# Kernel tuning notes

Measured on AMD Instinct MI355X. Metric: run time of the kernel, lower is better.

Reference implementation:

```python
import jax, jax.numpy as jnp
import numpy as np

B, T, H = 2, 2048, 1024
DFF = 4 * H        # dense_mlp hidden width
E = 8              # num_experts_temp
TOP_K = 2


def setup_inputs() -> dict:
    key = jax.random.key(0)
    ks = jax.random.split(key, 6)
    s_h = 1.0 / np.sqrt(H)
    s_f = 1.0 / np.sqrt(DFF)
    return {
        "hidden_states": jax.random.normal(ks[0], (B, T, H), dtype=jnp.float32),
        "router_w": jax.random.normal(ks[1], (E, H), dtype=jnp.float32) * s_h,
        "w1": jax.random.normal(ks[2], (E, H, DFF), dtype=jnp.float32) * s_h,
        "b1": jnp.zeros((E, DFF), dtype=jnp.float32),
        "w2": jax.random.normal(ks[3], (E, DFF, H), dtype=jnp.float32) * s_f,
        "b2": jnp.zeros((E, H), dtype=jnp.float32),
    }


def reference(hidden_states, router_w, w1, b1, w2, b2):
    # Router: [B,T,E]
    router_logits = jnp.einsum("bth,eh->bte", hidden_states, router_w)
    topk_vals, topk_idx = jax.lax.top_k(router_logits, TOP_K)        # [B,T,K]
    topk_w = jax.nn.softmax(topk_vals.astype(jnp.float32), axis=-1)
    topk_w = topk_w.astype(hidden_states.dtype)

    # Dense compute of ALL experts (faithful to the original module).
    h = jnp.einsum("bth,ehf->btef", hidden_states, w1) + b1          # [B,T,E,DFF]
    h = jax.nn.gelu(h)
    expert_out = jnp.einsum("btef,efh->bteh", h, w2) + b2            # [B,T,E,H]

    # Gather top-k experts per token and mix.
    topk_out = jnp.take_along_axis(expert_out, topk_idx[..., None], axis=2)  # [B,T,K,H]
    mixed = jnp.sum(topk_out * topk_w[..., None], axis=2)            # [B,T,H]
    return mixed
```

## Files before the change

### kernel.cpp

```cpp
#include <hip/hip_runtime.h>
#include <hip/hip_bf16.h>
#include <stdint.h>

#define AS1 __attribute__((address_space(1)))
#define AS3 __attribute__((address_space(3)))

typedef __bf16 bf16x8 __attribute__((ext_vector_type(8)));
typedef float floatx4 __attribute__((ext_vector_type(4)));

static constexpr int NTOK = 4096;
static constexpr int H    = 1024;
static constexpr int DFF  = 4096;
static constexpr int E    = 8;
static constexpr int BN   = 128;
static constexpr int RBMAX = 72;

static constexpr size_t OFF_WS     = 0;
static constexpr size_t OFF_XCS    = 67108864;
static constexpr size_t OFF_HS     = 85983232;
static constexpr size_t OFF_P1     = 161480704;
static constexpr size_t OFF_RTIDX  = 180355072;
static constexpr size_t OFF_RTW    = 180387840;
static constexpr size_t OFF_PTOK   = 180420608;
static constexpr size_t OFF_PW     = 180457472;
static constexpr size_t OFF_TOKPOS = 180494336;
static constexpr size_t OFF_CNT    = 180527104;
static constexpr size_t WS_NEED    = 180527232;

__device__ __forceinline__ unsigned short f2bf(float f) {
    __bf16 b = (__bf16)f;
    return __builtin_bit_cast(unsigned short, b);
}
__device__ __forceinline__ float bf2f(unsigned short u) {
    unsigned int v = ((unsigned int)u) << 16;
    return __builtin_bit_cast(float, v);
}

__device__ __forceinline__ void gload16(const void* g, void* l) {
    __builtin_amdgcn_global_load_lds((AS1 void*)g, (AS3 void*)l, 16, 0, 0);
}

__global__ __launch_bounds__(256) void k_router(const float* __restrict__ x,
                                                const float* __restrict__ rw,
                                                int* __restrict__ rt_idx,
                                                float* __restrict__ rt_w,
                                                int* __restrict__ counts) {
    const int wv = threadIdx.x >> 6, ln = threadIdx.x & 63;
    const int t = blockIdx.x * 4 + wv;
    const float* xr = x + (size_t)t * H + ln * 4;
    float4 xv[4];
#pragma unroll
    for (int c = 0; c < 4; ++c) xv[c] = *(const float4*)(xr + c * 256);
    float lg[E];
#pragma unroll
    for (int e = 0; e < E; ++e) {
        const float* rr = rw + (size_t)e * H + ln * 4;
        float acc = 0.f;
#pragma unroll
        for (int c = 0; c < 4; ++c) {
            float4 rv = *(const float4*)(rr + c * 256);
            acc += xv[c].x * rv.x + xv[c].y * rv.y + xv[c].z * rv.z + xv[c].w * rv.w;
        }
#pragma unroll
        for (int s = 32; s > 0; s >>= 1) acc += __shfl_xor(acc, s, 64);
        lg[e] = acc;
    }
    if (ln == 0) {
        int i0 = 0; float v0 = lg[0];
#pragma unroll
        for (int e = 1; e < E; ++e) if (lg[e] > v0) { v0 = lg[e]; i0 = e; }
        int i1 = -1; float v1 = -INFINITY;
#pragma unroll
        for (int e = 0; e < E; ++e) if (e != i0 && lg[e] > v1) { v1 = lg[e]; i1 = e; }
        float e1 = expf(v1 - v0);
        float inv = 1.f / (1.f + e1);
        rt_idx[2 * t] = i0; rt_idx[2 * t + 1] = i1;
        rt_w[2 * t] = inv;  rt_w[2 * t + 1] = e1 * inv;
        atomicAdd(&counts[i0], 1);
        atomicAdd(&counts[i1], 1);
    }
}

__global__ void k_offsets(const int* __restrict__ counts, int* __restrict__ offs) {
    if (threadIdx.x == 0) {
        int o = 0;
        for (int e = 0; e < E; ++e) { offs[e] = o; o += (counts[e] + 127) & ~127; }
        offs[E] = o;
    }
}

__global__ __launch_bounds__(256) void k_scatter(const int* __restrict__ rt_idx,
                                                 const float* __restrict__ rt_w,
                                                 const int* __restrict__ offs,
                                                 int* __restrict__ cursors,
                                                 int* __restrict__ pair_tok,
                                                 float* __restrict__ pair_w,
                                                 int* __restrict__ tok_pos) {
    int t = blockIdx.x * 256 + threadIdx.x;
    if (t >= NTOK) return;
    for (int k = 0; k < 2; ++k) {
        int e = rt_idx[2 * t + k];
        int p = atomicAdd(&cursors[e], 1);
        int pos = offs[e] + p;
        pair_tok[pos] = t;
        pair_w[pos] = rt_w[2 * t + k];
        tok_pos[2 * t + k] = pos;
    }
}

__global__ __launch_bounds__(256) void k_gather(const float* __restrict__ x,
                                                const int* __restrict__ offs,
                                                const int* __restrict__ counts,
                                                const int* __restrict__ pair_tok,
                                                unsigned short* __restrict__ xcs) {
    int pos = blockIdx.x;
    if (pos >= offs[E]) return;
    int e = 0;
    while (e < E - 1 && pos >= offs[e + 1]) ++e;
    bool valid = (pos - offs[e]) < counts[e];
    int tok = valid ? pair_tok[pos] : 0;
    int k0 = threadIdx.x * 4;
    float4 xv = valid ? *(const float4*)(x + (size_t)tok * H + k0)
                      : make_float4(0.f, 0.f, 0.f, 0.f);
    ushort4 o;
    o.x = f2bf(xv.x); o.y = f2bf(xv.y); o.z = f2bf(xv.z); o.w = f2bf(xv.w);
    int rb = pos >> 7, m = pos & 127;
    size_t idx = (((size_t)(rb * 32 + (k0 >> 5)) * 128 + m) * 32) + (((k0 >> 3) & 3) << 3) + (k0 & 7);
    *(ushort4*)(xcs + idx) = o;
}

template <int K, int N>
__global__ __launch_bounds__(256) void k_convert(const float* __restrict__ w,
                                                 unsigned short* __restrict__ ws) {
    constexpr int KB = K / 32, NB = N / 64;
    int bid = blockIdx.x;
    int nb = bid % NB, kb = (bid / NB) % KB, e = bid / (NB * KB);
    int kq = threadIdx.x & 3, nl = threadIdx.x >> 2;
    int n = nb * 64 + nl;
    const float* src = w + ((size_t)e * K + kb * 32 + kq * 8) * N + n;
    union { unsigned short us[8]; uint4 v; } u;
#pragma unroll
    for (int j = 0; j < 8; ++j) u.us[j] = f2bf(src[(size_t)j * N]);
    size_t oct = ((size_t)(e * KB + kb) * N + n) * 4 + kq;
    *(uint4*)(ws + oct * 8) = u.v;
}

__global__ __launch_bounds__(256) void k_gemm1(const unsigned short* __restrict__ Xc,
                                               const unsigned short* __restrict__ W1s,
                                               const int* __restrict__ offs,
                                               const float* __restrict__ b1,
                                               unsigned short* __restrict__ Hs) {
    constexpr int KB = H / 32;
    constexpr int MP = 36;
    const int rb = blockIdx.y;
    if (rb * 128 >= offs[E]) return;
    int e = 0;
    while (e < E - 1 && rb * 128 >= offs[e + 1]) ++e;
    const int n0 = blockIdx.x * BN;

    __shared__ unsigned short smem[4 * 128 * MP];
    unsigned short* lds_a = smem;
    unsigned short* lds_b = smem + 4096;

    const int tid = threadIdx.x;
    const int wv = tid >> 6, ln = tid & 63;
    const int quad = ln >> 4, lr = ln & 15;
    const int wm = (wv & 1) * 64, wn = (wv >> 1) * 64;

    floatx4 acc[4][4];
#pragma unroll
    for (int i = 0; i < 4; ++i)
#pragma unroll
        for (int j = 0; j < 4; ++j) acc[i][j] = (floatx4){0.f, 0.f, 0.f, 0.f};

    const unsigned short* Atile = Xc + (size_t)rb * KB * 4096;
    const unsigned short* Btile = W1s + ((size_t)e * KB * DFF + n0) * 32;

    for (int kb = 0; kb < KB; ++kb) {
        __syncthreads();
        const unsigned short* a_src = Atile + (size_t)kb * 4096 + (wv * 2) * 512 + ln * 8;
        const unsigned short* b_src = Btile + (size_t)kb * DFF * 32 + (wv * 2) * 512 + ln * 8;
#pragma unroll
        for (int c = 0; c < 2; ++c) {
            gload16(a_src + c * 512, &lds_a[(wv * 2 + c) * 512]);
            gload16(b_src + c * 512, &lds_b[(wv * 2 + c) * 512]);
        }
        __syncthreads();
        bf16x8 af[4], bg[4];
#pragma unroll
        for (int i = 0; i < 4; ++i) {
            af[i] = *(const bf16x8*)(lds_a + (wm + i * 16 + lr) * 32 + quad * 8);
            bg[i] = *(const bf16x8*)(lds_b + (wn + i * 16 + lr) * 32 + quad * 8);
        }
#pragma unroll
        for (int i = 0; i < 4; ++i)
#pragma unroll
            for (int j = 0; j < 4; ++j)
                acc[i][j] = __builtin_amdgcn_mfma_f32_16x16x32_bf16(af[i], bg[j], acc[i][j], 0, 0, 0);
    }

    float bj[4];
#pragma unroll
    for (int j = 0; j < 4; ++j) bj[j] = b1[(size_t)e * DFF + n0 + wn + j * 16 + lr];
    __syncthreads();
#pragma unroll
    for (int j = 0; j < 4; ++j) {
        const int fl = wn + j * 16 + lr;
        const int fb = fl >> 5, f5 = fl & 31;
        unsigned short* dst = smem + fb * (128 * MP) + f5;
#pragma unroll
        for (int i = 0; i < 4; ++i) {
#pragma unroll
            for (int r = 0; r < 4; ++r) {
                const int m = wm + i * 16 + quad * 4 + r;
                float v = acc[i][j][r] + bj[j];
                float u = 0.79788456080286535588f * (v + 0.044715f * v * v * v);
                float ez = __expf(2.f * u);
                float g = v * (1.f - 1.f / (ez + 1.f));
                dst[m * MP] = f2bf(g);
            }
        }
    }
    __syncthreads();
    const size_t hsbase = ((size_t)rb * 128 + (n0 >> 5)) * 4096;
#pragma unroll
    for (int it = 0; it < 8; ++it) {
        const int g = (it * 256 + tid) * 8;
        const int fb = g >> 12, rem = g & 4095, m = rem >> 5, f5 = rem & 31;
        const unsigned short* s = smem + fb * (128 * MP) + m * MP + f5;
        uint2 lo = *(const uint2*)s;
        uint2 hi = *(const uint2*)(s + 4);
        *(uint4*)(Hs + hsbase + (size_t)g) = make_uint4(lo.x, lo.y, hi.x, hi.y);
    }
}

__global__ __launch_bounds__(256) void k_gemm2(const unsigned short* __restrict__ Hs,
                                               const unsigned short* __restrict__ W2s,
                                               const int* __restrict__ offs,
                                               const float* __restrict__ b2,
                                               unsigned short* __restrict__ P0,
                                               unsigned short* __restrict__ P1) {
    constexpr int KB = DFF / 32;
    constexpr int KBS = KB / 2;
    const int rb = blockIdx.y;
    if (rb * 128 >= offs[E]) return;
    int e = 0;
    while (e < E - 1 && rb * 128 >= offs[e + 1]) ++e;
    const int ks = blockIdx.z;
    const int n0 = blockIdx.x * BN;

    __shared__ unsigned short smem[8192];
    unsigned short* lds_a = smem;
    unsigned short* lds_b = smem + 4096;

    const int tid = threadIdx.x;
    const int wv = tid >> 6, ln = tid & 63;
    const int quad = ln >> 4, lr = ln & 15;
    const int wm = (wv & 1) * 64, wn = (wv >> 1) * 64;

    floatx4 acc[4][4];
#pragma unroll
    for (int i = 0; i < 4; ++i)
#pragma unroll
        for (int j = 0; j < 4; ++j) acc[i][j] = (floatx4){0.f, 0.f, 0.f, 0.f};

    const unsigned short* Atile = Hs + (size_t)rb * KB * 4096;
    const unsigned short* Btile = W2s + ((size_t)e * KB * H + n0) * 32;

    for (int kb = ks * KBS; kb < ks * KBS + KBS; ++kb) {
        __syncthreads();
        const unsigned short* a_src = Atile + (size_t)kb * 4096 + (wv * 2) * 512 + ln * 8;
        const unsigned short* b_src = Btile + (size_t)kb * H * 32 + (wv * 2) * 512 + ln * 8;
#pragma unroll
        for (int c = 0; c < 2; ++c) {
            gload16(a_src + c * 512, &lds_a[(wv * 2 + c) * 512]);
            gload16(b_src + c * 512, &lds_b[(wv * 2 + c) * 512]);
        }
        __syncthreads();
        bf16x8 af[4], bg[4];
#pragma unroll
        for (int i = 0; i < 4; ++i) {
            af[i] = *(const bf16x8*)(lds_a + (wm + i * 16 + lr) * 32 + quad * 8);
            bg[i] = *(const bf16x8*)(lds_b + (wn + i * 16 + lr) * 32 + quad * 8);
        }
#pragma unroll
        for (int i = 0; i < 4; ++i)
#pragma unroll
            for (int j = 0; j < 4; ++j)
                acc[i][j] = __builtin_amdgcn_mfma_f32_16x16x32_bf16(af[i], bg[j], acc[i][j], 0, 0, 0);
    }

    float bj[4];
#pragma unroll
    for (int j = 0; j < 4; ++j)
        bj[j] = (ks == 0) ? b2[(size_t)e * H + n0 + wn + j * 16 + lr] : 0.f;
    unsigned short* P = ks ? P1 : P0;
#pragma unroll
    for (int i = 0; i < 4; ++i) {
#pragma unroll
        for (int r = 0; r < 4; ++r) {
            const int m = wm + i * 16 + quad * 4 + r;
            unsigned short* row = P + (size_t)(rb * 128 + m) * H + n0;
#pragma unroll
            for (int j = 0; j < 4; ++j)
                row[wn + j * 16 + lr] = f2bf(acc[i][j][r] + bj[j]);
        }
    }
}

__global__ __launch_bounds__(256) void k_mix(const unsigned short* __restrict__ P0,
                                             const unsigned short* __restrict__ P1,
                                             const int* __restrict__ tok_pos,
                                             const float* __restrict__ rt_w,
                                             float* __restrict__ out) {
    const int t = blockIdx.x;
    const int c = threadIdx.x * 4;
    const int p0 = tok_pos[2 * t], p1 = tok_pos[2 * t + 1];
    const float w0 = rt_w[2 * t], w1 = rt_w[2 * t + 1];
    ushort4 a0 = *(const ushort4*)(P0 + (size_t)p0 * H + c);
    ushort4 a1 = *(const ushort4*)(P1 + (size_t)p0 * H + c);
    ushort4 b0 = *(const ushort4*)(P0 + (size_t)p1 * H + c);
    ushort4 b1 = *(const ushort4*)(P1 + (size_t)p1 * H + c);
    float4 o;
    o.x = w0 * (bf2f(a0.x) + bf2f(a1.x)) + w1 * (bf2f(b0.x) + bf2f(b1.x));
    o.y = w0 * (bf2f(a0.y) + bf2f(a1.y)) + w1 * (bf2f(b0.y) + bf2f(b1.y));
    o.z = w0 * (bf2f(a0.z) + bf2f(a1.z)) + w1 * (bf2f(b0.z) + bf2f(b1.z));
    o.w = w0 * (bf2f(a0.w) + bf2f(a1.w)) + w1 * (bf2f(b0.w) + bf2f(b1.w));
    *(float4*)(out + (size_t)t * H + c) = o;
}

extern "C" void kernel_launch(void* const* d_in, const int* in_sizes, int n_in,
                              void* d_out, int out_size, void* d_ws, size_t ws_size,
                              hipStream_t stream) {
    const float* x  = (const float*)d_in[0];
    const float* rw = (const float*)d_in[1];
    const float* w1 = (const float*)d_in[2];
    const float* b1 = (const float*)d_in[3];
    const float* w2 = (const float*)d_in[4];
    const float* b2 = (const float*)d_in[5];
    float* out = (float*)d_out;
    char* ws = (char*)d_ws;
    if (ws_size < WS_NEED) return;

    unsigned short* Ws   = (unsigned short*)(ws + OFF_WS);
    unsigned short* XcS  = (unsigned short*)(ws + OFF_XCS);
    unsigned short* Hs   = (unsigned short*)(ws + OFF_HS);
    unsigned short* P1   = (unsigned short*)(ws + OFF_P1);
    int*   rt_idx   = (int*)(ws + OFF_RTIDX);
    float* rt_w     = (float*)(ws + OFF_RTW);
    int*   pair_tok = (int*)(ws + OFF_PTOK);
    float* pair_w   = (float*)(ws + OFF_PW);
    int*   tok_pos  = (int*)(ws + OFF_TOKPOS);
    int*   cnt      = (int*)(ws + OFF_CNT);
    int*   cur      = cnt + 8;
    int*   offs     = cnt + 16;

    hipMemsetAsync(cnt, 0, 128, stream);

    k_router<<<NTOK / 4, 256, 0, stream>>>(x, rw, rt_idx, rt_w, cnt);
    k_offsets<<<1, 64, 0, stream>>>(cnt, offs);
    k_scatter<<<NTOK / 256, 256, 0, stream>>>(rt_idx, rt_w, offs, cur, pair_tok, pair_w, tok_pos);
    k_gather<<<9216, 256, 0, stream>>>(x, offs, cnt, pair_tok, XcS);

    k_convert<H, DFF><<<8 * (H / 32) * (DFF / 64), 256, 0, stream>>>(w1, Ws);
    k_gemm1<<<dim3(DFF / BN, RBMAX), 256, 0, stream>>>(XcS, Ws, offs, b1, Hs);

    k_convert<DFF, H><<<8 * (DFF / 32) * (H / 64), 256, 0, stream>>>(w2, Ws);
    k_gemm2<<<dim3(H / BN, RBMAX, 2), 256, 0, stream>>>(Hs, Ws, offs, b2, XcS, P1);

    k_mix<<<NTOK, 256, 0, stream>>>(XcS, P1, tok_pos, rt_w, out);
}
```

Measured before the change: 689.8 us.

## Double-buffer LDS in grouped GEMMs and remap grid to expert-slot ordering

Both grouped GEMM kernels now prefetch the next K-tile into a second LDS buffer while computing the current one. This drops one barrier per iteration and overlaps global loads with MFMA work. The launch grid becomes 1D, with expert as the fastest-varying index and a fixed 16 row-block slots per expert, so concurrent blocks spread across experts' weights. The cost is doubled LDS usage in gemm2 and a fixed slot cap that assumes no expert exceeds 16*128 padded rows.

```diff
diff --git a/kernel.cpp b/kernel.cpp
--- a/kernel.cpp
+++ b/kernel.cpp
@@ -12,8 +12,7 @@
 static constexpr int H    = 1024;
 static constexpr int DFF  = 4096;
 static constexpr int E    = 8;
-static constexpr int BN   = 128;
-static constexpr int RBMAX = 72;
+static constexpr int SLOTS = 16;
 
 static constexpr size_t OFF_WS     = 0;
 static constexpr size_t OFF_XCS    = 67108864;
@@ -152,15 +151,17 @@
                                                unsigned short* __restrict__ Hs) {
     constexpr int KB = H / 32;
     constexpr int MP = 36;
-    const int rb = blockIdx.y;
-    if (rb * 128 >= offs[E]) return;
-    int e = 0;
-    while (e < E - 1 && rb * 128 >= offs[e + 1]) ++e;
-    const int n0 = blockIdx.x * BN;
+    const int bid = blockIdx.x;
+    const int e = bid & 7;
+    const int r = bid >> 3;
+    const int slot = r & (SLOTS - 1);
+    const int nb = r >> 4;
+    const int padcnt = offs[e + 1] - offs[e];
+    if (slot * 128 >= padcnt) return;
+    const int rb = (offs[e] >> 7) + slot;
+    const int n0 = nb * 128;
 
     __shared__ unsigned short smem[4 * 128 * MP];
-    unsigned short* lds_a = smem;
-    unsigned short* lds_b = smem + 4096;
 
     const int tid = threadIdx.x;
     const int wv = tid >> 6, ln = tid & 63;
@@ -173,24 +174,36 @@
 #pragma unroll
         for (int j = 0; j < 4; ++j) acc[i][j] = (floatx4){0.f, 0.f, 0.f, 0.f};
 
-    const unsigned short* Atile = Xc + (size_t)rb * KB * 4096;
-    const unsigned short* Btile = W1s + ((size_t)e * KB * DFF + n0) * 32;
-
+    const unsigned short* a_base = Xc + (size_t)rb * KB * 4096 + wv * 1024 + ln * 8;
+    const unsigned short* b_base = W1s + ((size_t)e * KB * DFF + n0) * 32 + wv * 1024 + ln * 8;
+
+    {
+        unsigned short* la = smem, *lb = smem + 4096;
+        gload16(a_base,        la + wv * 1024);
+        gload16(a_base + 512,  la + wv * 1024 + 512);
+        gload16(b_base,        lb + wv * 1024);
+        gload16(b_base + 512,  lb + wv * 1024 + 512);
+    }
     for (int kb = 0; kb < KB; ++kb) {
+        const int p = kb & 1;
         __syncthreads();
-        const unsigned short* a_src = Atile + (size_t)kb * 4096 + (wv * 2) * 512 + ln * 8;
-        const unsigned short* b_src = Btile + (size_t)kb * DFF * 32 + (wv * 2) * 512 + ln * 8;
-#pragma unroll
-        for (int c = 0; c < 2; ++c) {
-            gload16(a_src + c * 512, &lds_a[(wv * 2 + c) * 512]);
-            gload16(b_src + c * 512, &lds_b[(wv * 2 + c) * 512]);
-        }
-        __syncthreads();
+        if (kb + 1 < KB) {
+            unsigned short* la = smem + (p ^ 1) * 8192;
+            unsigned short* lb = la + 4096;
+            const unsigned short* as = a_base + (size_t)(kb + 1) * 4096;
+            const unsigned short* bs = b_base + (size_t)(kb + 1) * DFF * 32;
+            gload16(as,       la + wv * 1024);
+            gload16(as + 512, la + wv * 1024 + 512);
+            gload16(bs,       lb + wv * 1024);
+            gload16(bs + 512, lb + wv * 1024 + 512);
+        }
+        const unsigned short* la = smem + p * 8192;
+        const unsigned short* lb = la + 4096;
         bf16x8 af[4], bg[4];
 #pragma unroll
         for (int i = 0; i < 4; ++i) {
-            af[i] = *(const bf16x8*)(lds_a + (wm + i * 16 + lr) * 32 + quad * 8);
-            bg[i] = *(const bf16x8*)(lds_b + (wn + i * 16 + lr) * 32 + quad * 8);
+            af[i] = *(const bf16x8*)(la + (wm + i * 16 + lr) * 32 + quad * 8);
+            bg[i] = *(const bf16x8*)(lb + (wn + i * 16 + lr) * 32 + quad * 8);
         }
 #pragma unroll
         for (int i = 0; i < 4; ++i)
@@ -211,9 +224,9 @@
 #pragma unroll
         for (int i = 0; i < 4; ++i) {
 #pragma unroll
-            for (int r = 0; r < 4; ++r) {
-                const int m = wm + i * 16 + quad * 4 + r;
-                float v = acc[i][j][r] + bj[j];
+            for (int rr = 0; rr < 4; ++rr) {
+                const int m = wm + i * 16 + quad * 4 + rr;
+                float v = acc[i][j][rr] + bj[j];
                 float u = 0.79788456080286535588f * (v + 0.044715f * v * v * v);
                 float ez = __expf(2.f * u);
                 float g = v * (1.f - 1.f / (ez + 1.f));
@@ -242,16 +255,18 @@
                                                unsigned short* __restrict__ P1) {
     constexpr int KB = DFF / 32;
     constexpr int KBS = KB / 2;
-    const int rb = blockIdx.y;
-    if (rb * 128 >= offs[E]) return;
-    int e = 0;
-    while (e < E - 1 && rb * 128 >= offs[e + 1]) ++e;
-    const int ks = blockIdx.z;
-    const int n0 = blockIdx.x * BN;
-
-    __shared__ unsigned short smem[8192];
-    unsigned short* lds_a = smem;
-    unsigned short* lds_b = smem + 4096;
+    const int bid = blockIdx.x;
+    const int e = bid & 7;
+    const int r = bid >> 3;
+    const int slot = r & (SLOTS - 1);
+    const int nb = (r >> 4) & 7;
+    const int ks = r >> 7;
+    const int padcnt = offs[e + 1] - offs[e];
+    if (slot * 128 >= padcnt) return;
+    const int rb = (offs[e] >> 7) + slot;
+    const int n0 = nb * 128;
+
+    __shared__ unsigned short smem[16384];
 
     const int tid = threadIdx.x;
     const int wv = tid >> 6, ln = tid & 63;
@@ -264,24 +279,37 @@
 #pragma unroll
         for (int j = 0; j < 4; ++j) acc[i][j] = (floatx4){0.f, 0.f, 0.f, 0.f};
 
-    const unsigned short* Atile = Hs + (size_t)rb * KB * 4096;
-    const unsigned short* Btile = W2s + ((size_t)e * KB * H + n0) * 32;
-
-    for (int kb = ks * KBS; kb < ks * KBS + KBS; ++kb) {
+    const int kb0 = ks * KBS;
+    const unsigned short* a_base = Hs + ((size_t)rb * KB + kb0) * 4096 + wv * 1024 + ln * 8;
+    const unsigned short* b_base = W2s + (((size_t)e * KB + kb0) * H + n0) * 32 + wv * 1024 + ln * 8;
+
+    {
+        unsigned short* la = smem, *lb = smem + 4096;
+        gload16(a_base,        la + wv * 1024);
+        gload16(a_base + 512,  la + wv * 1024 + 512);
+        gload16(b_base,        lb + wv * 1024);
+        gload16(b_base + 512,  lb + wv * 1024 + 512);
+    }
+    for (int kb = 0; kb < KBS; ++kb) {
+        const int p = kb & 1;
         __syncthreads();
-        const unsigned short* a_src = Atile + (size_t)kb * 4096 + (wv * 2) * 512 + ln * 8;
-        const unsigned short* b_src = Btile + (size_t)kb * H * 32 + (wv * 2) * 512 + ln * 8;
-#pragma unroll
-        for (int c = 0; c < 2; ++c) {
-            gload16(a_src + c * 512, &lds_a[(wv * 2 + c) * 512]);
-            gload16(b_src + c * 512, &lds_b[(wv * 2 + c) * 512]);
-        }
-        __syncthreads();
+        if (kb + 1 < KBS) {
+            unsigned short* la = smem + (p ^ 1) * 8192;
+            unsigned short* lb = la + 4096;
+            const unsigned short* as = a_base + (size_t)(kb + 1) * 4096;
+            const unsigned short* bs = b_base + (size_t)(kb + 1) * H * 32;
+            gload16(as,       la + wv * 1024);
+            gload16(as + 512, la + wv * 1024 + 512);
+            gload16(bs,       lb + wv * 1024);
+            gload16(bs + 512, lb + wv * 1024 + 512);
+        }
+        const unsigned short* la = smem + p * 8192;
+        const unsigned short* lb = la + 4096;
         bf16x8 af[4], bg[4];
 #pragma unroll
         for (int i = 0; i < 4; ++i) {
-            af[i] = *(const bf16x8*)(lds_a + (wm + i * 16 + lr) * 32 + quad * 8);
-            bg[i] = *(const bf16x8*)(lds_b + (wn + i * 16 + lr) * 32 + quad * 8);
+            af[i] = *(const bf16x8*)(la + (wm + i * 16 + lr) * 32 + quad * 8);
+            bg[i] = *(const bf16x8*)(lb + (wn + i * 16 + lr) * 32 + quad * 8);
         }
 #pragma unroll
         for (int i = 0; i < 4; ++i)
@@ -298,12 +326,12 @@
 #pragma unroll
     for (int i = 0; i < 4; ++i) {
 #pragma unroll
-        for (int r = 0; r < 4; ++r) {
-            const int m = wm + i * 16 + quad * 4 + r;
+        for (int rr = 0; rr < 4; ++rr) {
+            const int m = wm + i * 16 + quad * 4 + rr;
             unsigned short* row = P + (size_t)(rb * 128 + m) * H + n0;
 #pragma unroll
             for (int j = 0; j < 4; ++j)
-                row[wn + j * 16 + lr] = f2bf(acc[i][j][r] + bj[j]);
+                row[wn + j * 16 + lr] = f2bf(acc[i][j][rr] + bj[j]);
         }
     }
 }
@@ -363,10 +391,10 @@
     k_gather<<<9216, 256, 0, stream>>>(x, offs, cnt, pair_tok, XcS);
 
     k_convert<H, DFF><<<8 * (H / 32) * (DFF / 64), 256, 0, stream>>>(w1, Ws);
-    k_gemm1<<<dim3(DFF / BN, RBMAX), 256, 0, stream>>>(XcS, Ws, offs, b1, Hs);
+    k_gemm1<<<E * SLOTS * (DFF / 128), 256, 0, stream>>>(XcS, Ws, offs, b1, Hs);
 
     k_convert<DFF, H><<<8 * (DFF / 32) * (H / 64), 256, 0, stream>>>(w2, Ws);
-    k_gemm2<<<dim3(H / BN, RBMAX, 2), 256, 0, stream>>>(Hs, Ws, offs, b2, XcS, P1);
+    k_gemm2<<<E * SLOTS * (H / 128) * 2, 256, 0, stream>>>(Hs, Ws, offs, b2, XcS, P1);
 
     k_mix<<<NTOK, 256, 0, stream>>>(XcS, P1, tok_pos, rt_w, out);
 }
```

New measurement: 707.6 us. +2.6%, slower.
